# Performance work log

Hardware: AMD Instinct MI355X
Metric: run time of the kernel (lower is better)

## Reference

```python
import jax, jax.numpy as jnp
import numpy as np

B = 4; D = H = W = 28; C = 192; NH = 6; WS = 7; SS = 3
L = D * H * W; N = WS ** 3; HD = C // NH


def _rel_index():
    c = np.stack(np.meshgrid(np.arange(WS), np.arange(WS), np.arange(WS), indexing='ij')).reshape(3, -1)
    r = c[:, :, None] - c[:, None, :] + (WS - 1)
    return jnp.asarray(r[0] * (2 * WS - 1) ** 2 + r[1] * (2 * WS - 1) + r[2])  # (N,N)


def _attn_mask():
    img = np.zeros((D, H, W), np.float32)
    sl = (slice(0, -WS), slice(-WS, -SS), slice(-SS, None))
    cnt = 0
    for d in sl:
        for h in sl:
            for w in sl:
                img[d, h, w] = cnt; cnt += 1
    mw = img.reshape(D // WS, WS, H // WS, WS, W // WS, WS).transpose(0, 2, 4, 1, 3, 5).reshape(-1, N)
    am = mw[:, None, :] - mw[:, :, None]
    return jnp.asarray(np.where(am != 0, -100.0, 0.0).astype(np.float32))  # (nW,N,N)

REL_IDX = _rel_index()
ATTN_MASK = _attn_mask()


def _ln(x, g, b):
    m = x.mean(-1, keepdims=True)
    v = ((x - m) ** 2).mean(-1, keepdims=True)
    return (x - m) / jnp.sqrt(v + 1e-5) * g + b


def _window_partition(x):  # (B,D,H,W,C) -> (B*nW, N, C)
    x = x.reshape(B, D // WS, WS, H // WS, WS, W // WS, WS, C)
    return x.transpose(0, 1, 3, 5, 2, 4, 6, 7).reshape(-1, N, C)


def _window_reverse(w):  # (B*nW, N, C) -> (B,D,H,W,C)
    x = w.reshape(B, D // WS, H // WS, W // WS, WS, WS, WS, C)
    return x.transpose(0, 1, 4, 2, 5, 3, 6, 7).reshape(B, D, H, W, C)


def setup_inputs() -> dict:
    key = jax.random.key(0)
    ks = jax.random.split(key, 8)
    s = 0.02
    return {
        'x': jax.random.normal(ks[0], (B, L, C), jnp.float32),
        'norm1_g': jnp.ones((C,), jnp.float32), 'norm1_b': jnp.zeros((C,), jnp.float32),
        'qkv_w': jax.random.normal(ks[1], (3 * C, C), jnp.float32) * s,
        'qkv_b': jnp.zeros((3 * C,), jnp.float32),
        'proj_w': jax.random.normal(ks[2], (C, C), jnp.float32) * s,
        'proj_b': jnp.zeros((C,), jnp.float32),
        'rel_table': jax.random.normal(ks[3], ((2 * WS - 1) ** 3, NH), jnp.float32) * s,
        'norm2_g': jnp.ones((C,), jnp.float32), 'norm2_b': jnp.zeros((C,), jnp.float32),
        'fc1_w': jax.random.normal(ks[4], (4 * C, C), jnp.float32) * s,
        'fc1_b': jnp.zeros((4 * C,), jnp.float32),
        'fc2_w': jax.random.normal(ks[5], (C, 4 * C), jnp.float32) * s,
        'fc2_b': jnp.zeros((C,), jnp.float32),
    }


def reference(x, norm1_g, norm1_b, qkv_w, qkv_b, proj_w, proj_b, rel_table,
              norm2_g, norm2_b, fc1_w, fc1_b, fc2_w, fc2_b):
    shortcut = x
    h = _ln(x, norm1_g, norm1_b).reshape(B, D, H, W, C)
    h = jnp.roll(h, (-SS, -SS, -SS), axis=(1, 2, 3))
    xw = _window_partition(h)                                  # (B_, N, C)
    B_ = xw.shape[0]
    qkv = (xw @ qkv_w.T + qkv_b).reshape(B_, N, 3, NH, HD).transpose(2, 0, 3, 1, 4)
    q, k, v = qkv[0], qkv[1], qkv[2]                           # (B_, NH, N, HD)
    attn = jnp.einsum('bhnd,bhmd->bhnm', q * (HD ** -0.5), k)
    bias = rel_table[REL_IDX].transpose(2, 0, 1)               # (NH, N, N)
    attn = attn + bias[None]
    nW = ATTN_MASK.shape[0]
    attn = (attn.reshape(B, nW, NH, N, N) + ATTN_MASK[None, :, None]).reshape(B_, NH, N, N)
    attn = jax.nn.softmax(attn, axis=-1)
    out = jnp.einsum('bhnm,bhmd->bhnd', attn, v).transpose(0, 2, 1, 3).reshape(B_, N, C)
    out = out @ proj_w.T + proj_b
    h = _window_reverse(out)
    h = jnp.roll(h, (SS, SS, SS), axis=(1, 2, 3)).reshape(B, L, C)
    x = shortcut + h
    y = _ln(x, norm2_g, norm2_b)
    y = jax.nn.gelu(y @ fc1_w.T + fc1_b, approximate=False)
    return x + (y @ fc2_w.T + fc2_b)
```

## Files before the change

kernel.cpp:

```cpp
#include <hip/hip_runtime.h>

#define DEV __device__ __forceinline__

typedef __bf16 bf16x8 __attribute__((ext_vector_type(8)));
typedef float f32x4 __attribute__((ext_vector_type(4)));

DEV float bflo(unsigned int u) { union { unsigned int x; float f; } c; c.x = u << 16; return c.f; }
DEV unsigned short f2bf(float f) {
  union { float f; unsigned int u; } c; c.f = f;
  unsigned int u = c.u;
  return (unsigned short)((u + 0x7fffu + ((u >> 16) & 1u)) >> 16);
}
DEV unsigned int pkbf(float a, float b) {
  unsigned int r;
  asm("v_cvt_pk_bf16_f32 %0, %1, %2" : "=v"(r) : "v"(a), "v"(b));
  return r;
}
DEV float gelu_fast(float y) {
  float y2 = y * y;
  float z = y * fmaf(y2, 0.10294348f, 2.30220842f);
  float e = __builtin_amdgcn_exp2f(z);
  float r = __builtin_amdgcn_rcpf(e + 1.0f);
  return fmaf(-y, r, y);
}

DEV void gload16(const void* g, void* l) {
  __builtin_amdgcn_global_load_lds((const __attribute__((address_space(1))) void*)g,
                                   (__attribute__((address_space(3))) void*)l, 16, 0, 0);
}

__global__ __launch_bounds__(256) void wconv_all(const float* __restrict__ s0,
                                                 const float* __restrict__ s1,
                                                 const float* __restrict__ s2,
                                                 const float* __restrict__ s3,
                                                 unsigned short* __restrict__ dst) {
  int i = blockIdx.x * 256 + threadIdx.x;
  const float* src; int off, real;
  if (i < 122880)      { src = s0; off = i;          real = 110592; }
  else if (i < 172032) { src = s1; off = i - 122880; real = 36864; }
  else if (i < 319488) { src = s2; off = i - 172032; real = 147456; }
  else                 { src = s3; off = i - 319488; real = 147456; }
  dst[i] = (off < real) ? f2bf(src[off]) : (unsigned short)0;
}

__global__ __launch_bounds__(256) void bmt_kernel(const float* __restrict__ rel_table,
                                                  unsigned short* __restrict__ bmt4) {
  int wth = blockIdx.x;
  int wt = wth / 6, h = wth - wt * 6;
  int r = blockIdx.y;
  unsigned short* row = bmt4 + (((size_t)wth * 88 + r) * 352) * 4;
  for (int q = threadIdx.x; q < 352; q += 256) {
    int mb_q = 0, cls_q = 0;
    bool qv = q < 343;
    if (qv) {
      int ii_q = q / 49, rem_q = q - ii_q * 49;
      int jj_q = rem_q / 7, ww_q = rem_q - jj_q * 7;
      mb_q = ii_q * 169 + jj_q * 13 + ww_q;
      int cd_q = (wt & 4) ? (ii_q < 4 ? 1 : 2) : 0;
      int ch_q = (wt & 2) ? (jj_q < 4 ? 1 : 2) : 0;
      int cw_q = (wt & 1) ? (ww_q < 4 ? 1 : 2) : 0;
      cls_q = cd_q * 9 + ch_q * 3 + cw_q;
    }
    unsigned short ov[4];
#pragma unroll
    for (int i = 0; i < 4; i++) {
      int kk = 4 * r + i;
      float v;
      if (kk >= 343) v = -30000.f;
      else if (!qv) v = 0.f;
      else {
        int ii_k = kk / 49, rem_k = kk - ii_k * 49;
        int jj_k = rem_k / 7, ww_k = rem_k - jj_k * 7;
        int mb_k = ii_k * 169 + jj_k * 13 + ww_k;
        int cd_k = (wt & 4) ? (ii_k < 4 ? 1 : 2) : 0;
        int ch_k = (wt & 2) ? (jj_k < 4 ? 1 : 2) : 0;
        int cw_k = (wt & 1) ? (ww_k < 4 ? 1 : 2) : 0;
        int cls_k = cd_k * 9 + ch_k * 3 + cw_k;
        v = rel_table[(mb_q - mb_k + 1098) * 6 + h] * 1.4426950408889634f;
        if (cls_q != cls_k) v -= 144.26950408889634f;
      }
      ov[i] = f2bf(v);
    }
    unsigned int lo = (unsigned)ov[0] | ((unsigned)ov[1] << 16);
    unsigned int hi = (unsigned)ov[2] | ((unsigned)ov[3] << 16);
    *(uint2*)(row + q * 4) = make_uint2(lo, hi);
  }
}

__global__ __launch_bounds__(256) void ln_kernel(const float* __restrict__ x,
                                                 const float* __restrict__ g,
                                                 const float* __restrict__ b,
                                                 unsigned short* __restrict__ out) {
  int row = (blockIdx.x << 2) + (threadIdx.x >> 6);
  int lane = threadIdx.x & 63;
  int w_ = row / 343, n_ = row - w_ * 343;
  int bb = w_ >> 6, wrem = w_ & 63;
  int wd = wrem >> 4, wh = (wrem >> 2) & 3, ww = wrem & 3;
  int ii = n_ / 49, rem = n_ - ii * 49;
  int jj = rem / 7, kk = rem - jj * 7;
  int d = wd * 7 + ii + 3; if (d >= 28) d -= 28;
  int hh = wh * 7 + jj + 3; if (hh >= 28) hh -= 28;
  int wb = ww * 7 + kk + 3; if (wb >= 28) wb -= 28;
  const float* xr = x + ((size_t)bb * 21952 + (d * 28 + hh) * 28 + wb) * 192;
  float v0 = xr[lane], v1 = xr[lane + 64], v2 = xr[lane + 128];
  float s = v0 + v1 + v2;
  float sq = v0 * v0 + v1 * v1 + v2 * v2;
#pragma unroll
  for (int o = 32; o > 0; o >>= 1) {
    s += __shfl_xor(s, o, 64);
    sq += __shfl_xor(sq, o, 64);
  }
  float mean = s * (1.0f / 192.0f);
  float var = sq * (1.0f / 192.0f) - mean * mean;
  float rstd = rsqrtf(var + 1e-5f);
  unsigned short* orow = out + (size_t)row * 192;
  orow[lane]       = f2bf((v0 - mean) * rstd * g[lane] + b[lane]);
  orow[lane + 64]  = f2bf((v1 - mean) * rstd * g[lane + 64] + b[lane + 64]);
  orow[lane + 128] = f2bf((v2 - mean) * rstd * g[lane + 128] + b[lane + 128]);
}

__global__ __launch_bounds__(256) void gemm_qkv(
    const unsigned short* __restrict__ A, const unsigned short* __restrict__ W,
    const float* __restrict__ bias,
    unsigned short* __restrict__ oq, unsigned short* __restrict__ okk,
    unsigned short* __restrict__ ov) {
  __shared__ __align__(16) unsigned short As[2][128 * 64];
  __shared__ __align__(16) unsigned short Bs[2][128 * 64];
  const int K = 192;
  const int orig = blockIdx.x;
  const int xcd = orig & 7, off = orig >> 3;
  const int wgid = (xcd < 6 ? xcd * 429 : 2574 + (xcd - 6) * 428) + off;
  const int by = wgid / 5, bx = wgid - by * 5;
  const int bm = by << 7, bn = bx << 7;

  const int tid = threadIdx.x;
  const int lane = tid & 63;
  const int wv = tid >> 6;
  const int wr = wv >> 1, wc = wv & 1;
  const int l15 = lane & 15, l4 = lane >> 4;
  const int srow = lane >> 3;
  const int scole = ((lane & 7) ^ srow) << 3;

  f32x4 acc[4][4];
#pragma unroll
  for (int a = 0; a < 4; a++)
#pragma unroll
    for (int b2 = 0; b2 < 4; b2++) acc[a][b2] = (f32x4){0.f, 0.f, 0.f, 0.f};

  auto stage = [&](int kt, int buf) {
#pragma unroll
    for (int i = 0; i < 4; i++) {
      int c = (i << 2) + wv;
      int row = (c << 3) + srow;
      gload16(A + (size_t)(bm + row) * K + (kt << 6) + scole, &As[buf][c << 9]);
      gload16(W + (size_t)(bn + row) * K + (kt << 6) + scole, &Bs[buf][c << 9]);
    }
  };

  stage(0, 0);
  int cur = 0;
  for (int kt = 0; kt < 3; ++kt) {
    if (kt < 2) {
      stage(kt + 1, cur ^ 1);
      asm volatile("s_waitcnt vmcnt(8)" ::: "memory");
    } else {
      asm volatile("s_waitcnt vmcnt(0)" ::: "memory");
    }
    __builtin_amdgcn_s_barrier();
    __builtin_amdgcn_sched_barrier(0);
#pragma unroll
    for (int ks = 0; ks < 2; ks++) {
      bf16x8 af[4], bfr[4];
#pragma unroll
      for (int fm = 0; fm < 4; fm++) {
        int r = (wr << 6) + (fm << 4) + l15;
        int c = (ks << 2) + l4;
        af[fm] = *(const bf16x8*)(&As[cur][(r << 6) + ((c ^ (r & 7)) << 3)]);
      }
#pragma unroll
      for (int fn = 0; fn < 4; fn++) {
        int r = (wc << 6) + (fn << 4) + l15;
        int c = (ks << 2) + l4;
        bfr[fn] = *(const bf16x8*)(&Bs[cur][(r << 6) + ((c ^ (r & 7)) << 3)]);
      }
#pragma unroll
      for (int fm = 0; fm < 4; fm++)
#pragma unroll
        for (int fn = 0; fn < 4; fn++)
          acc[fm][fn] = __builtin_amdgcn_mfma_f32_16x16x32_bf16(bfr[fn], af[fm], acc[fm][fn], 0, 0, 0);
    }
    if (kt < 2) {
      __builtin_amdgcn_sched_barrier(0);
      __builtin_amdgcn_s_barrier();
      cur ^= 1;
    }
  }

#pragma unroll
  for (int fm = 0; fm < 4; fm++) {
    int gr = bm + (wr << 6) + (fm << 4) + l15;
    int w_ = gr / 343, n_ = gr - w_ * 343;
#pragma unroll
    for (int fn = 0; fn < 4; fn++) {
      int gc0 = bn + (wc << 6) + (fn << 4) + (l4 << 2);
      if (gc0 < 576) {
        float4 bv = *(const float4*)(bias + gc0);
        float v0 = acc[fm][fn][0] + bv.x, v1 = acc[fm][fn][1] + bv.y;
        float v2 = acc[fm][fn][2] + bv.z, v3 = acc[fm][fn][3] + bv.w;
        int which = gc0 / 192;
        int cc3 = gc0 - which * 192;
        int hh2 = cc3 >> 5, dd0 = cc3 & 31;
        size_t offo = ((size_t)(w_ * 6 + hh2) * 343 + n_) * 32 + dd0;
        if (which == 0) {
          const float sc = 0.17677669529663687f * 1.4426950408889634f;
          *(uint2*)(oq + offo) = make_uint2(pkbf(v0 * sc, v1 * sc), pkbf(v2 * sc, v3 * sc));
        } else if (which == 1) {
          *(uint2*)(okk + offo) = make_uint2(pkbf(v0, v1), pkbf(v2, v3));
        } else {
          *(uint2*)(ov + offo) = make_uint2(pkbf(v0, v1), pkbf(v2, v3));
        }
      }
    }
  }
}

__global__ __launch_bounds__(256, 3) void proj_mlp(
    const unsigned short* __restrict__ A,
    const unsigned short* __restrict__ Wp, const float* __restrict__ bp,
    const float* __restrict__ x,
    const float* __restrict__ g2, const float* __restrict__ b2,
    const unsigned short* __restrict__ W1, const float* __restrict__ b1,
    const unsigned short* __restrict__ W2, const float* __restrict__ b2b,
    float* __restrict__ out) {
  __shared__ __align__(16) char smem[41984];
  unsigned short* As = (unsigned short*)smem;
  unsigned short* Hs = (unsigned short*)(smem + 24576);
  float* red = (float*)(smem + 24576);

  const int tid = threadIdx.x, lane = tid & 63, wv = tid >> 6;
  const int l15 = lane & 15, l4 = lane >> 4;
  const int bm = blockIdx.x << 6;

  int orow[4];
#pragma unroll
  for (int fm = 0; fm < 4; fm++) {
    int gr = bm + (fm << 4) + l15;
    int w_ = gr / 343, n_ = gr - w_ * 343;
    int bb = w_ >> 6, wrem = w_ & 63;
    int wd = wrem >> 4, wh = (wrem >> 2) & 3, ww = wrem & 3;
    int ii = n_ / 49, rem = n_ - ii * 49;
    int jj = rem / 7, kk = rem - jj * 7;
    int d = wd * 7 + ii + 3; if (d >= 28) d -= 28;
    int hh = wh * 7 + jj + 3; if (hh >= 28) hh -= 28;
    int wb = ww * 7 + kk + 3; if (wb >= 28) wb -= 28;
    orow[fm] = ((bb * 21952 + (d * 28 + hh) * 28 + wb) * 192);
  }

#pragma unroll
  for (int i = 0; i < 6; i++) {
    int idx = (i << 8) + tid;
    int r = idx / 24, c = idx - r * 24;
    gload16(A + (size_t)(bm + r) * 192 + ((c ^ (r & 7)) << 3), As + r * 192 + (c << 3));
  }
  asm volatile("s_waitcnt vmcnt(0)" ::: "memory");
  __builtin_amdgcn_s_barrier();

  float4 xv[4][3];
#pragma unroll
  for (int fm = 0; fm < 4; fm++)
#pragma unroll
    for (int fn = 0; fn < 3; fn++) {
      int gc0 = wv * 48 + (fn << 4) + (l4 << 2);
      xv[fm][fn] = *(const float4*)(x + (size_t)orow[fm] + gc0);
    }

  f32x4 acc[4][3];
#pragma unroll
  for (int a = 0; a < 4; a++)
#pragma unroll
    for (int b_ = 0; b_ < 3; b_++) acc[a][b_] = (f32x4){0.f, 0.f, 0.f, 0.f};
#pragma unroll
  for (int ks = 0; ks < 6; ks++) {
    bf16x8 af[4], wpf[3];
#pragma unroll
    for (int fm = 0; fm < 4; fm++) {
      int r = (fm << 4) + l15;
      int ch = (ks << 2) + l4;
      af[fm] = *(const bf16x8*)(As + r * 192 + ((ch ^ (r & 7)) << 3));
    }
#pragma unroll
    for (int fn = 0; fn < 3; fn++) {
      int rr = wv * 48 + (fn << 4) + l15;
      wpf[fn] = *(const bf16x8*)(Wp + (size_t)rr * 192 + (ks << 5) + (l4 << 3));
    }
#pragma unroll
    for (int fm = 0; fm < 4; fm++)
#pragma unroll
      for (int fn = 0; fn < 3; fn++)
        acc[fm][fn] = __builtin_amdgcn_mfma_f32_16x16x32_bf16(wpf[fn], af[fm], acc[fm][fn], 0, 0, 0);
  }

  float ps[4], psq[4];
#pragma unroll
  for (int fm = 0; fm < 4; fm++) {
    float s = 0.f, sq = 0.f;
#pragma unroll
    for (int fn = 0; fn < 3; fn++) {
      int gc0 = wv * 48 + (fn << 4) + (l4 << 2);
      float4 bv = *(const float4*)(bp + gc0);
      acc[fm][fn][0] += bv.x + xv[fm][fn].x;
      acc[fm][fn][1] += bv.y + xv[fm][fn].y;
      acc[fm][fn][2] += bv.z + xv[fm][fn].z;
      acc[fm][fn][3] += bv.w + xv[fm][fn].w;
#pragma unroll
      for (int i = 0; i < 4; i++) {
        float v = acc[fm][fn][i];
        s += v; sq += v * v;
      }
    }
    ps[fm] = s; psq[fm] = sq;
  }
#pragma unroll
  for (int fm = 0; fm < 4; fm++) {
    ps[fm] += __shfl_xor(ps[fm], 16, 64);
    ps[fm] += __shfl_xor(ps[fm], 32, 64);
    psq[fm] += __shfl_xor(psq[fm], 16, 64);
    psq[fm] += __shfl_xor(psq[fm], 32, 64);
  }
  __syncthreads();
  if (l4 == 0) {
#pragma unroll
    for (int fm = 0; fm < 4; fm++) {
      int tr = (fm << 4) + l15;
      red[tr * 8 + wv] = ps[fm];
      red[tr * 8 + 4 + wv] = psq[fm];
    }
  }
  __syncthreads();
  if (tid < 64) {
    float s = red[tid * 8] + red[tid * 8 + 1] + red[tid * 8 + 2] + red[tid * 8 + 3];
    float sq = red[tid * 8 + 4] + red[tid * 8 + 5] + red[tid * 8 + 6] + red[tid * 8 + 7];
    float mean = s * (1.0f / 192.0f);
    float var = sq * (1.0f / 192.0f) - mean * mean;
    red[tid * 8] = mean;
    red[tid * 8 + 1] = rsqrtf(var + 1e-5f);
  }
  __syncthreads();
  unsigned int xnb[4][3][2];
#pragma unroll
  for (int fm = 0; fm < 4; fm++) {
    int tr = (fm << 4) + l15;
    float mean = red[tr * 8], rstd = red[tr * 8 + 1];
#pragma unroll
    for (int fn = 0; fn < 3; fn++) {
      int gc0 = wv * 48 + (fn << 4) + (l4 << 2);
      float4 gv = *(const float4*)(g2 + gc0);
      float4 b2v = *(const float4*)(b2 + gc0);
      float v0 = acc[fm][fn][0], v1 = acc[fm][fn][1];
      float v2 = acc[fm][fn][2], v3 = acc[fm][fn][3];
      xnb[fm][fn][0] = pkbf(v0, v1);
      xnb[fm][fn][1] = pkbf(v2, v3);
      float y0 = (v0 - mean) * rstd * gv.x + b2v.x;
      float y1 = (v1 - mean) * rstd * gv.y + b2v.y;
      float y2 = (v2 - mean) * rstd * gv.z + b2v.z;
      float y3 = (v3 - mean) * rstd * gv.w + b2v.w;
      int ch = gc0 >> 3;
      *(uint2*)(As + tr * 192 + ((ch ^ (tr & 7)) << 3) + (gc0 & 7)) =
          make_uint2(pkbf(y0, y1), pkbf(y2, y3));
    }
  }
  __syncthreads();

  f32x4 acc2[4][3];
#pragma unroll
  for (int a = 0; a < 4; a++)
#pragma unroll
    for (int b_ = 0; b_ < 3; b_++) acc2[a][b_] = (f32x4){0.f, 0.f, 0.f, 0.f};

  for (int cc = 0; cc < 6; cc++) {
    f32x4 acc1[4][2];
#pragma unroll
    for (int a = 0; a < 4; a++) {
      acc1[a][0] = (f32x4){0.f, 0.f, 0.f, 0.f};
      acc1[a][1] = (f32x4){0.f, 0.f, 0.f, 0.f};
    }
#pragma unroll
    for (int ks = 0; ks < 6; ks++) {
      bf16x8 af[4], w1f[2];
#pragma unroll
      for (int fm = 0; fm < 4; fm++) {
        int r = (fm << 4) + l15;
        int ch = (ks << 2) + l4;
        af[fm] = *(const bf16x8*)(As + r * 192 + ((ch ^ (r & 7)) << 3));
      }
#pragma unroll
      for (int fn = 0; fn < 2; fn++) {
        int hrow = (cc << 7) + (wv << 5) + (fn << 4) + l15;
        w1f[fn] = *(const bf16x8*)(W1 + (size_t)hrow * 192 + (ks << 5) + (l4 << 3));
      }
#pragma unroll
      for (int fm = 0; fm < 4; fm++)
#pragma unroll
        for (int fn = 0; fn < 2; fn++)
          acc1[fm][fn] = __builtin_amdgcn_mfma_f32_16x16x32_bf16(w1f[fn], af[fm], acc1[fm][fn], 0, 0, 0);
    }
    __syncthreads();
#pragma unroll
    for (int fm = 0; fm < 4; fm++) {
      int r = (fm << 4) + l15;
#pragma unroll
      for (int fn = 0; fn < 2; fn++) {
        int hc = (wv << 5) + (fn << 4) + (l4 << 2);
        float4 bv = *(const float4*)(b1 + (cc << 7) + hc);
        float g0 = gelu_fast(acc1[fm][fn][0] + bv.x);
        float g1 = gelu_fast(acc1[fm][fn][1] + bv.y);
        float g2_ = gelu_fast(acc1[fm][fn][2] + bv.z);
        float g3 = gelu_fast(acc1[fm][fn][3] + bv.w);
        *(uint2*)(Hs + r * 136 + hc) = make_uint2(pkbf(g0, g1), pkbf(g2_, g3));
      }
    }
    __syncthreads();
#pragma unroll
    for (int ks = 0; ks < 4; ks++) {
      bf16x8 hf[4], w2f[3];
#pragma unroll
      for (int fm = 0; fm < 4; fm++) {
        int r = (fm << 4) + l15;
        hf[fm] = *(const bf16x8*)(Hs + r * 136 + (ks << 5) + (l4 << 3));
      }
#pragma unroll
      for (int fn = 0; fn < 3; fn++) {
        int j = wv * 48 + (fn << 4) + l15;
        w2f[fn] = *(const bf16x8*)(W2 + (size_t)j * 768 + (cc << 7) + (ks << 5) + (l4 << 3));
      }
#pragma unroll
      for (int fm = 0; fm < 4; fm++)
#pragma unroll
        for (int fn = 0; fn < 3; fn++)
          acc2[fm][fn] = __builtin_amdgcn_mfma_f32_16x16x32_bf16(w2f[fn], hf[fm], acc2[fm][fn], 0, 0, 0);
    }
  }

#pragma unroll
  for (int fm = 0; fm < 4; fm++) {
#pragma unroll
    for (int fn = 0; fn < 3; fn++) {
      int gc0 = wv * 48 + (fn << 4) + (l4 << 2);
      float4 bv = *(const float4*)(b2b + gc0);
      float4 o;
      o.x = acc2[fm][fn][0] + bv.x + bflo(xnb[fm][fn][0] & 0xffffu);
      o.y = acc2[fm][fn][1] + bv.y + bflo(xnb[fm][fn][0] >> 16);
      o.z = acc2[fm][fn][2] + bv.z + bflo(xnb[fm][fn][1] & 0xffffu);
      o.w = acc2[fm][fn][3] + bv.w + bflo(xnb[fm][fn][1] >> 16);
      *(float4*)(out + (size_t)orow[fm] + gc0) = o;
    }
  }
}

__global__ __launch_bounds__(256) void attn_mfma(const unsigned short* __restrict__ q,
                                                 const unsigned short* __restrict__ k,
                                                 const unsigned short* __restrict__ v,
                                                 const unsigned short* __restrict__ bmt4,
                                                 unsigned short* __restrict__ out) {
  __shared__ __align__(16) unsigned short Ks[352 * 32];
  __shared__ __align__(16) unsigned short Vt[32 * 360];

  const int blk = blockIdx.x;
  const int h_ = blk >> 8;
  const int idx = blk & 255;
  const int cums[8] = {0, 108, 144, 180, 192, 228, 240, 252};
  int c = (idx >= 108) + (idx >= 144) + (idx >= 180) + (idx >= 192) +
          (idx >= 228) + (idx >= 240) + (idx >= 252);
  int r0 = idx - cums[c];
  int sh = (c & 2) ? 1 : 3, sw = (c & 1) ? 1 : 3;
  int p = ((c & 4) ? 1 : 3) * sh * sw;
  int b = r0 / p, q2 = r0 - b * p;
  int wd, wh, ww;
  if (c & 4) wd = 3; else { wd = q2 / (sh * sw); q2 -= wd * sh * sw; }
  if (c & 2) wh = 3; else { wh = q2 / sw; q2 -= wh * sw; }
  ww = (c & 1) ? 3 : q2;
  const int w_ = b * 64 + wd * 16 + wh * 4 + ww;
  const int wt = c;
  const int blkqkv = w_ * 6 + h_;

  const int t = threadIdx.x, lane = t & 63, wv = t >> 6;
  const int l15 = lane & 15, l4 = lane >> 4;
  const unsigned short* Qb = q + (size_t)blkqkv * (343 * 32);
  const unsigned short* Kb = k + (size_t)blkqkv * (343 * 32);
  const unsigned short* Vb = v + (size_t)blkqkv * (343 * 32);
  const unsigned short* bm4 = bmt4 + ((size_t)(wt * 6 + h_) * 88) * 352 * 4;

  for (int cc = t; cc < 1408; cc += 256) {
    int r = cc >> 2, ch = cc & 3;
    int swc = ch ^ ((r >> 1) & 3);
    uint4 val = make_uint4(0, 0, 0, 0);
    if (r < 343) val = *(const uint4*)(Kb + r * 32 + ch * 8);
    *(uint4*)(Ks + r * 32 + swc * 8) = val;
  }
#pragma unroll
  for (int ch = 0; ch < 4; ch++) {
    for (int n = t; n < 343; n += 256) {
      union { uint4 u4; unsigned short us[8]; } val;
      val.u4 = *(const uint4*)(Vb + n * 32 + ch * 8);
#pragma unroll
      for (int j = 0; j < 8; j++) Vt[(ch * 8 + j) * 360 + n] = val.us[j];
    }
  }
  for (int cc = t; cc < 288; cc += 256) {
    int d = cc / 9, n = 343 + (cc - d * 9);
    Vt[d * 360 + n] = 0;
  }
  __syncthreads();

  const int ksw = (l4 ^ ((l15 >> 1) & 3)) << 3;

  for (int tq = wv; tq < 22; tq += 4) {
    int qrow = tq * 16 + l15; if (qrow > 342) qrow = 342;
    bf16x8 qf = *(const bf16x8*)(Qb + qrow * 32 + l4 * 8);

    unsigned int u0[22], u1[22];
    float lsum = 0.f;
#pragma unroll
    for (int kt = 0; kt < 22; kt++) {
      bf16x8 kf = *(const bf16x8*)(Ks + (kt * 16 + l15) * 32 + ksw);
      f32x4 s = __builtin_amdgcn_mfma_f32_16x16x32_bf16(kf, qf, (f32x4){0.f, 0.f, 0.f, 0.f}, 0, 0, 0);
      const unsigned short* bp = bm4 + ((size_t)((kt << 2) + l4) * 352 + (tq << 4) + l15) * 4;
      uint2 bv = *(const uint2*)bp;
      float p0 = __builtin_amdgcn_exp2f(s[0] + bflo(bv.x & 0xffffu));
      float p1 = __builtin_amdgcn_exp2f(s[1] + bflo(bv.x >> 16));
      float p2 = __builtin_amdgcn_exp2f(s[2] + bflo(bv.y & 0xffffu));
      float p3 = __builtin_amdgcn_exp2f(s[3] + bflo(bv.y >> 16));
      lsum += (p0 + p1) + (p2 + p3);
      asm("v_cvt_pk_bf16_f32 %0, %1, %2" : "=v"(u0[kt]) : "v"(p0), "v"(p1));
      asm("v_cvt_pk_bf16_f32 %0, %1, %2" : "=v"(u1[kt]) : "v"(p2), "v"(p3));
    }
    lsum += __shfl_xor(lsum, 16, 64);
    lsum += __shfl_xor(lsum, 32, 64);
    float inv = 1.0f / lsum;

    f32x4 oacc0 = (f32x4){0.f, 0.f, 0.f, 0.f};
    f32x4 oacc1 = (f32x4){0.f, 0.f, 0.f, 0.f};
#pragma unroll
    for (int ck = 0; ck < 11; ck++) {
      unsigned int dw[4];
#pragma unroll
      for (int d = 0; d < 4; d++) {
        int src = l15 + 16 * ((d >> 1) + 2 * (l4 & 1));
        unsigned int x = __shfl((d & 1) ? u1[2 * ck] : u0[2 * ck], src, 64);
        unsigned int y = __shfl((d & 1) ? u1[2 * ck + 1] : u0[2 * ck + 1], src, 64);
        dw[d] = (l4 < 2) ? x : y;
      }
      union { unsigned int u[4]; bf16x8 v; } pc;
      pc.u[0] = dw[0]; pc.u[1] = dw[1]; pc.u[2] = dw[2]; pc.u[3] = dw[3];
      bf16x8 vf0 = *(const bf16x8*)(Vt + (size_t)l15 * 360 + ck * 32 + l4 * 8);
      bf16x8 vf1 = *(const bf16x8*)(Vt + (size_t)(16 + l15) * 360 + ck * 32 + l4 * 8);
      oacc0 = __builtin_amdgcn_mfma_f32_16x16x32_bf16(vf0, pc.v, oacc0, 0, 0, 0);
      oacc1 = __builtin_amdgcn_mfma_f32_16x16x32_bf16(vf1, pc.v, oacc1, 0, 0, 0);
    }

    int qg = tq * 16 + l15;
    if (qg < 343) {
      unsigned short* orow = out + ((size_t)w_ * 343 + qg) * 192 + h_ * 32;
      *(uint2*)(orow + (l4 << 2)) =
          make_uint2(pkbf(oacc0[0] * inv, oacc0[1] * inv), pkbf(oacc0[2] * inv, oacc0[3] * inv));
      *(uint2*)(orow + 16 + (l4 << 2)) =
          make_uint2(pkbf(oacc1[0] * inv, oacc1[1] * inv), pkbf(oacc1[2] * inv, oacc1[3] * inv));
    }
  }
}

extern "C" void kernel_launch(void* const* d_in, const int* in_sizes, int n_in,
                              void* d_out, int out_size, void* d_ws, size_t ws_size,
                              hipStream_t stream) {
  const float* x      = (const float*)d_in[0];
  const float* n1g    = (const float*)d_in[1];
  const float* n1b    = (const float*)d_in[2];
  const float* qkv_w  = (const float*)d_in[3];
  const float* qkv_b  = (const float*)d_in[4];
  const float* proj_w = (const float*)d_in[5];
  const float* proj_b = (const float*)d_in[6];
  const float* rel_t  = (const float*)d_in[7];
  const float* n2g    = (const float*)d_in[8];
  const float* n2b    = (const float*)d_in[9];
  const float* fc1_w  = (const float*)d_in[10];
  const float* fc1_b  = (const float*)d_in[11];
  const float* fc2_w  = (const float*)d_in[12];
  const float* fc2_b  = (const float*)d_in[13];

  char* ws = (char*)d_ws;
  if (ws_size < 147820032ull) return;
  unsigned short* WQKV  = (unsigned short*)(ws);
  unsigned short* WPROJ = (unsigned short*)(ws + 245760);
  unsigned short* WFC1  = (unsigned short*)(ws + 344064);
  unsigned short* WFC2  = (unsigned short*)(ws + 638976);
  unsigned short* XW    = (unsigned short*)(ws + 1032192);
  unsigned short* Q_    = (unsigned short*)(ws + 34750464);
  unsigned short* K_    = (unsigned short*)(ws + 68468736);
  unsigned short* V_    = (unsigned short*)(ws + 102187008);
  unsigned short* BMT4  = (unsigned short*)(ws + 135925248);
  float* OUT = (float*)d_out;

  wconv_all<<<2016, 256, 0, stream>>>(qkv_w, proj_w, fc1_w, fc2_w, WQKV);

  bmt_kernel<<<dim3(48, 88), 256, 0, stream>>>(rel_t, BMT4);

  ln_kernel<<<21952, 256, 0, stream>>>(x, n1g, n1b, XW);

  gemm_qkv<<<3430, 256, 0, stream>>>(XW, WQKV, qkv_b, Q_, K_, V_);

  attn_mfma<<<1536, 256, 0, stream>>>(Q_, K_, V_, BMT4, XW);

  proj_mlp<<<1372, 256, 0, stream>>>(XW, WPROJ, proj_b, x, n2g, n2b,
                                     WFC1, fc1_b, WFC2, fc2_b, OUT);
}
```

Baseline: 318.6 us.

## Shrink QKV GEMM K-tile, move residual load later, add wave priority hints

The QKV GEMM now stages 32-wide K tiles over six iterations instead of 64-wide tiles over three, with a 4-way XOR swizzle. This halves its shared memory and may raise occupancy, but it doubles the number of barriers. The proj_mlp kernel now loads the residual x inside the epilogue instead of prefetching it into registers, and its launch bound drops from 3 to 2 blocks per SM. The attention kernel wraps its MFMA/exp loops in s_setprio raises to favour waves in compute phases.

```diff
diff --git a/kernel.cpp b/kernel.cpp
--- a/kernel.cpp
+++ b/kernel.cpp
@@ -124,8 +124,8 @@
     const float* __restrict__ bias,
     unsigned short* __restrict__ oq, unsigned short* __restrict__ okk,
     unsigned short* __restrict__ ov) {
-  __shared__ __align__(16) unsigned short As[2][128 * 64];
-  __shared__ __align__(16) unsigned short Bs[2][128 * 64];
+  __shared__ __align__(16) unsigned short As[2][128 * 32];
+  __shared__ __align__(16) unsigned short Bs[2][128 * 32];
   const int K = 192;
   const int orig = blockIdx.x;
   const int xcd = orig & 7, off = orig >> 3;
@@ -138,8 +138,6 @@
   const int wv = tid >> 6;
   const int wr = wv >> 1, wc = wv & 1;
   const int l15 = lane & 15, l4 = lane >> 4;
-  const int srow = lane >> 3;
-  const int scole = ((lane & 7) ^ srow) << 3;
 
   f32x4 acc[4][4];
 #pragma unroll
@@ -149,39 +147,38 @@
 
   auto stage = [&](int kt, int buf) {
 #pragma unroll
-    for (int i = 0; i < 4; i++) {
-      int c = (i << 2) + wv;
-      int row = (c << 3) + srow;
-      gload16(A + (size_t)(bm + row) * K + (kt << 6) + scole, &As[buf][c << 9]);
-      gload16(W + (size_t)(bn + row) * K + (kt << 6) + scole, &Bs[buf][c << 9]);
+    for (int i = 0; i < 2; i++) {
+      int o = (i << 12) + (tid << 4);
+      int r = o >> 6;
+      int c = (o >> 4) & 3;
+      int sc = (c ^ (r & 3)) << 3;
+      gload16(A + (size_t)(bm + r) * K + kt * 32 + sc, &As[buf][o >> 1]);
+      gload16(W + (size_t)(bn + r) * K + kt * 32 + sc, &Bs[buf][o >> 1]);
     }
   };
 
   stage(0, 0);
   int cur = 0;
-  for (int kt = 0; kt < 3; ++kt) {
-    if (kt < 2) {
+  for (int kt = 0; kt < 6; ++kt) {
+    if (kt < 5) {
       stage(kt + 1, cur ^ 1);
-      asm volatile("s_waitcnt vmcnt(8)" ::: "memory");
+      asm volatile("s_waitcnt vmcnt(4)" ::: "memory");
     } else {
       asm volatile("s_waitcnt vmcnt(0)" ::: "memory");
     }
     __builtin_amdgcn_s_barrier();
     __builtin_amdgcn_sched_barrier(0);
-#pragma unroll
-    for (int ks = 0; ks < 2; ks++) {
+    {
       bf16x8 af[4], bfr[4];
 #pragma unroll
       for (int fm = 0; fm < 4; fm++) {
         int r = (wr << 6) + (fm << 4) + l15;
-        int c = (ks << 2) + l4;
-        af[fm] = *(const bf16x8*)(&As[cur][(r << 6) + ((c ^ (r & 7)) << 3)]);
+        af[fm] = *(const bf16x8*)(&As[cur][(r << 5) + ((l4 ^ (r & 3)) << 3)]);
       }
 #pragma unroll
       for (int fn = 0; fn < 4; fn++) {
         int r = (wc << 6) + (fn << 4) + l15;
-        int c = (ks << 2) + l4;
-        bfr[fn] = *(const bf16x8*)(&Bs[cur][(r << 6) + ((c ^ (r & 7)) << 3)]);
+        bfr[fn] = *(const bf16x8*)(&Bs[cur][(r << 5) + ((l4 ^ (r & 3)) << 3)]);
       }
 #pragma unroll
       for (int fm = 0; fm < 4; fm++)
@@ -189,7 +186,7 @@
         for (int fn = 0; fn < 4; fn++)
           acc[fm][fn] = __builtin_amdgcn_mfma_f32_16x16x32_bf16(bfr[fn], af[fm], acc[fm][fn], 0, 0, 0);
     }
-    if (kt < 2) {
+    if (kt < 5) {
       __builtin_amdgcn_sched_barrier(0);
       __builtin_amdgcn_s_barrier();
       cur ^= 1;
@@ -224,7 +221,7 @@
   }
 }
 
-__global__ __launch_bounds__(256, 3) void proj_mlp(
+__global__ __launch_bounds__(256, 2) void proj_mlp(
     const unsigned short* __restrict__ A,
     const unsigned short* __restrict__ Wp, const float* __restrict__ bp,
     const float* __restrict__ x,
@@ -265,15 +262,6 @@
   asm volatile("s_waitcnt vmcnt(0)" ::: "memory");
   __builtin_amdgcn_s_barrier();
 
-  float4 xv[4][3];
-#pragma unroll
-  for (int fm = 0; fm < 4; fm++)
-#pragma unroll
-    for (int fn = 0; fn < 3; fn++) {
-      int gc0 = wv * 48 + (fn << 4) + (l4 << 2);
-      xv[fm][fn] = *(const float4*)(x + (size_t)orow[fm] + gc0);
-    }
-
   f32x4 acc[4][3];
 #pragma unroll
   for (int a = 0; a < 4; a++)
@@ -308,10 +296,11 @@
     for (int fn = 0; fn < 3; fn++) {
       int gc0 = wv * 48 + (fn << 4) + (l4 << 2);
       float4 bv = *(const float4*)(bp + gc0);
-      acc[fm][fn][0] += bv.x + xv[fm][fn].x;
-      acc[fm][fn][1] += bv.y + xv[fm][fn].y;
-      acc[fm][fn][2] += bv.z + xv[fm][fn].z;
-      acc[fm][fn][3] += bv.w + xv[fm][fn].w;
+      float4 xv = *(const float4*)(x + (size_t)orow[fm] + gc0);
+      acc[fm][fn][0] += bv.x + xv.x;
+      acc[fm][fn][1] += bv.y + xv.y;
+      acc[fm][fn][2] += bv.z + xv.z;
+      acc[fm][fn][3] += bv.w + xv.w;
 #pragma unroll
       for (int i = 0; i < 4; i++) {
         float v = acc[fm][fn][i];
@@ -520,6 +509,7 @@
 
     unsigned int u0[22], u1[22];
     float lsum = 0.f;
+    __builtin_amdgcn_s_setprio(1);
 #pragma unroll
     for (int kt = 0; kt < 22; kt++) {
       bf16x8 kf = *(const bf16x8*)(Ks + (kt * 16 + l15) * 32 + ksw);
@@ -534,12 +524,14 @@
       asm("v_cvt_pk_bf16_f32 %0, %1, %2" : "=v"(u0[kt]) : "v"(p0), "v"(p1));
       asm("v_cvt_pk_bf16_f32 %0, %1, %2" : "=v"(u1[kt]) : "v"(p2), "v"(p3));
     }
+    __builtin_amdgcn_s_setprio(0);
     lsum += __shfl_xor(lsum, 16, 64);
     lsum += __shfl_xor(lsum, 32, 64);
     float inv = 1.0f / lsum;
 
     f32x4 oacc0 = (f32x4){0.f, 0.f, 0.f, 0.f};
     f32x4 oacc1 = (f32x4){0.f, 0.f, 0.f, 0.f};
+    __builtin_amdgcn_s_setprio(1);
 #pragma unroll
     for (int ck = 0; ck < 11; ck++) {
       unsigned int dw[4];
@@ -557,6 +549,7 @@
       oacc0 = __builtin_amdgcn_mfma_f32_16x16x32_bf16(vf0, pc.v, oacc0, 0, 0, 0);
       oacc1 = __builtin_amdgcn_mfma_f32_16x16x32_bf16(vf1, pc.v, oacc1, 0, 0, 0);
     }
+    __builtin_amdgcn_s_setprio(0);
 
     int qg = tq * 16 + l15;
     if (qg < 343) {
```

New measurement: 314.1 us. Within noise of the previous version (-1.4%).
